# Optimization experiments

Hardware: AMD Instinct MI355X
Metric: run time of the kernel (lower is better)

The kernel has to match this reference:

```python
import jax, jax.numpy as jnp
import numpy as np

B, N = 2, 256
IN_N = 32          # input node features
H = 8              # per-layer default num_heads (GAT does not override it)
HN, HE = 64, 64    # hidden node / edge features per head
DN, DE = HN * H, HE * H  # 512, 512
OUT_N = 32


def _gat_layer(nodes, edges, mask, Wn, bn, We, be, Wa):
    # nodes: [b,n,dn_in], edges: [b,n,n,de_in], mask: [b,n] bool
    nf = nodes @ Wn + bn                                   # [b,n,DN]
    ef = jnp.einsum('bije,ef->bijf', edges, We) + be       # [b,n,n,DE]
    q = nf @ Wa                                            # [b,n,H]
    qe = jnp.einsum('bijf,fh->bijh', ef, Wa)               # [b,n,n,H]
    sn = jnp.einsum('bik,bjk->bij', q, q) / np.float32(np.sqrt(HN))
    se = jnp.einsum('bik,bijk->bij', q, qe) / np.float32(np.sqrt(HE))
    m = mask[..., None]
    wn = jax.nn.softmax(sn * m, axis=-1)                   # [b,n,n]
    we = jax.nn.softmax(se * m, axis=-1)                   # [b,n,n]
    awn = jnp.einsum('bij,bik->bjk', wn, nf)               # [b,n,DN]
    agg_e = jnp.einsum('bij,bijk->bik', we, ef)            # [b,n,DE]
    upd_nodes = nf + awn + agg_e                           # [b,n,DN]
    upd_edges = ef + we[..., None] * ef + jnp.einsum('bij,bik->bijk', wn, nf)
    re = jax.nn.elu(upd_edges)                             # [b,n,n,DE]
    re = (re + jnp.swapaxes(re, 1, 2)) / 2
    return jax.nn.elu(upd_nodes), re


def setup_inputs() -> dict:
    key = jax.random.key(0)
    ks = jax.random.split(key, 16)
    s = 0.05
    return {
        'nodes': jax.random.normal(ks[0], (B, N, IN_N), jnp.float32),
        'edges': jax.random.normal(ks[1], (B, N, N), jnp.float32),
        'node_mask': jnp.ones((B, N), dtype=bool),
        # layer 1 params
        'Wn1': jax.random.normal(ks[2], (IN_N, DN), jnp.float32) * s,
        'bn1': jnp.zeros((DN,), jnp.float32),
        'We1': jax.random.normal(ks[3], (1, DE), jnp.float32) * s,
        'be1': jnp.zeros((DE,), jnp.float32),
        'Wa1': jax.random.normal(ks[4], (DN, H), jnp.float32) * s,
        # layer 2 params
        'Wn2': jax.random.normal(ks[5], (DN, DN), jnp.float32) * s,
        'bn2': jnp.zeros((DN,), jnp.float32),
        'We2': jax.random.normal(ks[6], (DE, DE), jnp.float32) * s,
        'be2': jnp.zeros((DE,), jnp.float32),
        'Wa2': jax.random.normal(ks[7], (DN, H), jnp.float32) * s,
        # final projections
        'Wfn': jax.random.normal(ks[8], (DN, OUT_N), jnp.float32) * s,
        'bfn': jnp.zeros((OUT_N,), jnp.float32),
        'Wfe': jax.random.normal(ks[9], (DE, 1), jnp.float32) * s,
        'bfe': jnp.zeros((1,), jnp.float32),
    }


def reference(nodes, edges, node_mask, Wn1, bn1, We1, be1, Wa1,
              Wn2, bn2, We2, be2, Wa2, Wfn, bfn, Wfe, bfe):
    e = edges[..., None]                      # [b,n,n,1]
    e = (e + jnp.swapaxes(e, 1, 2)) / 2       # symmetrize
    e = jax.nn.relu(e)
    n, e = _gat_layer(nodes, e, node_mask, Wn1, bn1, We1, be1, Wa1)
    n, e = _gat_layer(n, e, node_mask, Wn2, bn2, We2, be2, Wa2)
    out_nodes = jnp.tanh(n @ Wfn + bfn)                                   # [b,n,OUT_N]
    out_edges = jnp.tanh(jnp.einsum('bijf,fo->bijo', e, Wfe) + bfe)[..., 0]  # [b,n,n]
    return out_nodes, out_edges
```

## Files before the change

### kernel.cpp

```cpp
#include <hip/hip_runtime.h>
#include <hip/hip_bf16.h>
#include <stdint.h>


typedef __attribute__((ext_vector_type(8))) short short8v;
typedef __attribute__((ext_vector_type(4))) float f32x4;

#define AS1 __attribute__((address_space(1)))
#define AS3 __attribute__((address_space(3)))

__device__ __forceinline__ float eluf(float x) { return x > 0.f ? x : (__expf(x) - 1.f); }

__device__ __forceinline__ short f2bf(float x) {
  union { float f; unsigned u; } v; v.f = x;
  unsigned r = v.u + 0x7fffu + ((v.u >> 16) & 1u);
  return (short)(r >> 16);
}

template<int OP>
__device__ float blockRed256(float v, float* s4) {
#pragma unroll
  for (int o = 32; o; o >>= 1) { float t = __shfl_xor(v, o); v = OP ? fmaxf(v, t) : v + t; }
  int w = threadIdx.x >> 6;
  __syncthreads();
  if ((threadIdx.x & 63) == 0) s4[w] = v;
  __syncthreads();
  return OP ? fmaxf(fmaxf(s4[0], s4[1]), fmaxf(s4[2], s4[3]))
            : (s4[0] + s4[1] + s4[2] + s4[3]);
}

__global__ __launch_bounds__(256) void k0m(const float* __restrict__ We2,
    const float* __restrict__ Wa2, const float* __restrict__ We1,
    const float* __restrict__ be1, const float* __restrict__ be2,
    const float* __restrict__ Wa1, short* __restrict__ Bp, float* __restrict__ M2,
    float* __restrict__ u1, float* __restrict__ v1, float* __restrict__ vb2) {
  int bid = blockIdx.x;
  if (bid < 128) {
    int id = bid * 256 + threadIdx.x;
    int c = id >> 11; int rem = id & 2047; int g = rem >> 9; int n = rem & 511;
    short8v v;
#pragma unroll
    for (int e = 0; e < 8; e++) v[e] = f2bf(We2[(c * 32 + g * 8 + e) * 512 + n]);
    int pos = n * 4 + (g ^ ((n >> 1) & 3));
    *(short8v*)(Bp + (c * 2048 + pos) * 8) = v;
    return;
  }
  int lane = threadIdx.x & 63;
  int idx = (bid - 128) * 4 + (threadIdx.x >> 6);
  if (idx < 512) {
    float a[8] = {0, 0, 0, 0, 0, 0, 0, 0};
    for (int k0 = lane; k0 < 512; k0 += 64) {
      float wv = We2[idx * 512 + k0];
      const float* wa = Wa2 + k0 * 8;
#pragma unroll
      for (int h = 0; h < 8; h++) a[h] += wv * wa[h];
    }
#pragma unroll
    for (int h = 0; h < 8; h++) {
      float v = a[h];
      for (int o = 32; o; o >>= 1) v += __shfl_xor(v, o);
      if (lane == 0) M2[idx * 8 + h] = v;
    }
  } else if (idx < 515) {
    const float* src = (idx == 512) ? We1 : (idx == 513 ? be1 : be2);
    const float* Wa = (idx == 514) ? Wa2 : Wa1;
    float* dst = (idx == 512) ? u1 : (idx == 513 ? v1 : vb2);
    float a[8] = {0, 0, 0, 0, 0, 0, 0, 0};
    for (int f = lane; f < 512; f += 64) {
      float s = src[f];
#pragma unroll
      for (int h = 0; h < 8; h++) a[h] += s * Wa[f * 8 + h];
    }
#pragma unroll
    for (int h = 0; h < 8; h++) {
      float v = a[h];
      for (int o = 32; o; o >>= 1) v += __shfl_xor(v, o);
      if (lane == 0) dst[h] = v;
    }
  }
}

__global__ __launch_bounds__(512) void k1_nf1(const float* __restrict__ nodes,
    const float* __restrict__ Wn1, const float* __restrict__ bn1,
    const float* __restrict__ Wa1, float* __restrict__ nf1, float* __restrict__ q1) {
  __shared__ float nrow[32];
  __shared__ float qL[8];
  int bi = blockIdx.x; int f = threadIdx.x;
  if (f < 32) nrow[f] = nodes[bi * 32 + f];
  if (f < 8) qL[f] = 0.f;
  __syncthreads();
  float acc = bn1[f];
#pragma unroll 8
  for (int c = 0; c < 32; c++) acc += nrow[c] * Wn1[c * 512 + f];
  nf1[bi * 512 + f] = acc;
  const float* wa = Wa1 + f * 8;
#pragma unroll
  for (int h = 0; h < 8; h++) {
    float v = acc * wa[h];
    for (int o = 32; o; o >>= 1) v += __shfl_xor(v, o);
    if ((f & 63) == 0) atomicAdd(&qL[h], v);
  }
  __syncthreads();
  if (f < 8) q1[bi * 8 + f] = qL[f];
}

__global__ __launch_bounds__(256) void k2_l1attn(const float* __restrict__ edges,
    const float* __restrict__ q1, const float* __restrict__ u1, const float* __restrict__ v1,
    float* __restrict__ e0, float* __restrict__ wn1, float* __restrict__ we1,
    float* __restrict__ tt) {
  __shared__ float s4[4];
  int bi = blockIdx.x; int b = bi >> 8; int i = bi & 255; int j = threadIdx.x;
  float qi[8], qj[8];
#pragma unroll
  for (int h = 0; h < 8; h++) { qi[h] = q1[bi * 8 + h]; qj[h] = q1[(b * 256 + j) * 8 + h]; }
  float eij = edges[bi * 256 + j];
  float eji = edges[(b * 256 + j) * 256 + i];
  float e0v = fmaxf(0.f, 0.5f * (eij + eji));
  e0[bi * 256 + j] = e0v;
  float sn = 0.f, aI = 0.f, cI = 0.f;
#pragma unroll
  for (int h = 0; h < 8; h++) { sn += qi[h] * qj[h]; aI += qi[h] * u1[h]; cI += qi[h] * v1[h]; }
  sn *= 0.125f;
  float se = (aI * e0v + cI) * 0.125f;
  float mn = blockRed256<1>(sn, s4);
  float en = __expf(sn - mn);
  float sumn = blockRed256<0>(en, s4);
  float wnv = en / sumn; wn1[bi * 256 + j] = wnv;
  float me = blockRed256<1>(se, s4);
  float ee = __expf(se - me);
  float sume = blockRed256<0>(ee, s4);
  float wev = ee / sume; we1[bi * 256 + j] = wev;
  float t = blockRed256<0>(wev * e0v, s4);
  if (j == 0) tt[bi] = t;
}

__global__ __launch_bounds__(512) void k34(const float* __restrict__ nf1,
    const float* __restrict__ wn1, const float* __restrict__ tt,
    const float* __restrict__ We1, const float* __restrict__ be1,
    const float* __restrict__ Wn2, const float* __restrict__ bn2,
    const float* __restrict__ Wa2, const float* __restrict__ M2,
    const float* __restrict__ vb2, float* __restrict__ nf2, float* __restrict__ q2,
    float* __restrict__ p2, float* __restrict__ cst) {
  __shared__ float n1L[2][512];
  __shared__ float qL[2][8];
  int bx = blockIdx.x;
  int b = bx >> 7; int x0 = (bx & 127) * 2; int k = threadIdx.x;
  int g0 = b * 256 + x0;
  float a0 = 0.f, a1 = 0.f;
#pragma unroll 4
  for (int i = 0; i < 256; i++) {
    float nv = nf1[(size_t)(b * 256 + i) * 512 + k];
    a0 += wn1[(b * 256 + i) * 256 + x0] * nv;
    a1 += wn1[(b * 256 + i) * 256 + x0 + 1] * nv;
  }
  float w = We1[k], be = be1[k];
  n1L[0][k] = eluf(nf1[(size_t)g0 * 512 + k] + a0 + tt[g0] * w + be);
  n1L[1][k] = eluf(nf1[(size_t)(g0 + 1) * 512 + k] + a1 + tt[g0 + 1] * w + be);
  if (k < 16) qL[k >> 3][k & 7] = 0.f;
  __syncthreads();
  float acc0 = bn2[k], acc1 = bn2[k];
#pragma unroll 4
  for (int g = 0; g < 512; g++) {
    float wv = Wn2[g * 512 + k];
    acc0 += n1L[0][g] * wv; acc1 += n1L[1][g] * wv;
  }
  nf2[(size_t)g0 * 512 + k] = acc0;
  nf2[(size_t)(g0 + 1) * 512 + k] = acc1;
  const float* wa = Wa2 + k * 8;
#pragma unroll
  for (int h = 0; h < 8; h++) {
    float v0 = acc0 * wa[h], v1 = acc1 * wa[h];
    for (int o = 32; o; o >>= 1) { v0 += __shfl_xor(v0, o); v1 += __shfl_xor(v1, o); }
    if ((k & 63) == 0) { atomicAdd(&qL[0][h], v0); atomicAdd(&qL[1][h], v1); }
  }
  __syncthreads();
  float q0[8], q1v[8];
#pragma unroll
  for (int h = 0; h < 8; h++) { q0[h] = qL[0][h]; q1v[h] = qL[1][h]; }
  if (k < 8) { q2[g0 * 8 + k] = q0[k]; q2[(g0 + 1) * 8 + k] = q1v[k]; }
  float p0 = 0.f, p1 = 0.f; const float* m2 = M2 + k * 8;
#pragma unroll
  for (int h = 0; h < 8; h++) { p0 += m2[h] * q0[h]; p1 += m2[h] * q1v[h]; }
  p2[(size_t)g0 * 512 + k] = p0;
  p2[(size_t)(g0 + 1) * 512 + k] = p1;
  if (k == 0) {
    float c0 = 0.f, c1 = 0.f;
#pragma unroll
    for (int h = 0; h < 8; h++) { c0 += q0[h] * vb2[h]; c1 += q1v[h] * vb2[h]; }
    cst[g0] = c0; cst[g0 + 1] = c1;
  }
}

__global__ __launch_bounds__(256) void k5b_pairs(const float* __restrict__ nf1,
    const float* __restrict__ p2, const float* __restrict__ e0,
    const float* __restrict__ wn1, const float* __restrict__ we1,
    const float* __restrict__ We1, const float* __restrict__ be1,
    const float* __restrict__ cst, float* __restrict__ se2) {
  __shared__ float NI[16 * 132], NJ[16 * 132], PI[16 * 132], PJ[16 * 132];
  __shared__ float W1[128], B1[128];
  int bid = blockIdx.x; int b = bid & 1; int pr = bid >> 1;
  int I = 0;
  { int p = pr; while (p >= 16 - I) { p -= 16 - I; I++; } pr = p; }
  int J = I + pr;
  int I0 = I * 16, J0 = J * 16;
  int tid = threadIdx.x; int ii = tid & 15, jj = tid >> 4;
  int gi = b * 256 + I0 + ii, gj = b * 256 + J0 + jj;
  int ij = gi * 256 + (J0 + jj), ji = gj * 256 + (I0 + ii);
  float e0v = e0[ij];
  float s1 = 1.f + we1[ij], w1 = wn1[ij];
  float s2 = 1.f + we1[ji], w2 = wn1[ji];
  float dot1 = 0.f, dot2 = 0.f;
  for (int fc = 0; fc < 4; fc++) {
    __syncthreads();
    int f00 = fc * 128;
    for (int t = tid; t < 2048; t += 256) {
      int row = t >> 7, f = t & 127;
      NI[row * 132 + f] = nf1[(size_t)(b * 256 + I0 + row) * 512 + f00 + f];
      NJ[row * 132 + f] = nf1[(size_t)(b * 256 + J0 + row) * 512 + f00 + f];
      PI[row * 132 + f] = p2[(size_t)(b * 256 + I0 + row) * 512 + f00 + f];
      PJ[row * 132 + f] = p2[(size_t)(b * 256 + J0 + row) * 512 + f00 + f];
    }
    if (tid < 128) { W1[tid] = We1[f00 + tid]; B1[tid] = be1[f00 + tid]; }
    __syncthreads();
#pragma unroll 8
    for (int f = 0; f < 128; f += 4) {
      float4 niv = *(const float4*)&NI[ii * 132 + f];
      float4 njv = *(const float4*)&NJ[jj * 132 + f];
      float4 piv = *(const float4*)&PI[ii * 132 + f];
      float4 pjv = *(const float4*)&PJ[jj * 132 + f];
      float4 wv = *(const float4*)&W1[f];
      float4 bv = *(const float4*)&B1[f];
      float ni_[4] = {niv.x, niv.y, niv.z, niv.w};
      float nj_[4] = {njv.x, njv.y, njv.z, njv.w};
      float pi_[4] = {piv.x, piv.y, piv.z, piv.w};
      float pj_[4] = {pjv.x, pjv.y, pjv.z, pjv.w};
      float w_[4] = {wv.x, wv.y, wv.z, wv.w};
      float b_[4] = {bv.x, bv.y, bv.z, bv.w};
#pragma unroll
      for (int e = 0; e < 4; e++) {
        float ef = e0v * w_[e] + b_[e];
        float x1 = ef * s1 + w1 * ni_[e];
        float x2 = ef * s2 + w2 * nj_[e];
        float e1v = 0.5f * (eluf(x1) + eluf(x2));
        dot1 += e1v * pi_[e];
        dot2 += e1v * pj_[e];
      }
    }
  }
  se2[ij] = (dot1 + cst[gi]) * 0.125f;
  se2[ji] = (dot2 + cst[gj]) * 0.125f;
}

__global__ __launch_bounds__(256) void k5ac(const float* __restrict__ q2,
    const float* __restrict__ se2, float* __restrict__ wn2, float* __restrict__ we2) {
  __shared__ float s4[4];
  int bi = blockIdx.x; int b = bi >> 8; int j = threadIdx.x;
  float sn = 0.f;
#pragma unroll
  for (int h = 0; h < 8; h++) sn += q2[bi * 8 + h] * q2[(b * 256 + j) * 8 + h];
  sn *= 0.125f;
  float mn = blockRed256<1>(sn, s4);
  float en = __expf(sn - mn);
  float s = blockRed256<0>(en, s4);
  wn2[bi * 256 + j] = en / s;
  float se = se2[bi * 256 + j];
  float me = blockRed256<1>(se, s4);
  float ee = __expf(se - me);
  float s2 = blockRed256<0>(ee, s4);
  we2[bi * 256 + j] = ee / s2;
}

__global__ __launch_bounds__(256) void kz(const float* __restrict__ nf1,
    const float* __restrict__ e0, const float* __restrict__ wn1,
    const float* __restrict__ we1, const float* __restrict__ we2,
    const float* __restrict__ We1, const float* __restrict__ be1, float* __restrict__ Z) {
  __shared__ float e0L[256], s1L[256], w1L[256], s2L[256], w2L[256], weL[256];
  int bi = blockIdx.x; int b = bi >> 8; int i = bi & 255; int tid = threadIdx.x;
  e0L[tid] = e0[bi * 256 + tid];
  s1L[tid] = 1.f + we1[bi * 256 + tid];
  w1L[tid] = wn1[bi * 256 + tid];
  weL[tid] = we2[bi * 256 + tid];
  s2L[tid] = 1.f + we1[(b * 256 + tid) * 256 + i];
  w2L[tid] = wn1[(b * 256 + tid) * 256 + i];
  __syncthreads();
  int k0 = tid, k1 = tid + 256;
  float W0 = We1[k0], B0 = be1[k0], W1 = We1[k1], B1 = be1[k1];
  float ni0 = nf1[(size_t)bi * 512 + k0], ni1 = nf1[(size_t)bi * 512 + k1];
  float z0 = 0.f, z1 = 0.f;
  const float* nfb = nf1 + (size_t)b * 256 * 512;
#pragma unroll 2
  for (int j = 0; j < 256; j++) {
    float e0v = e0L[j], s1 = s1L[j], w1 = w1L[j], s2 = s2L[j], w2 = w2L[j], we = weL[j];
    const float* nj = nfb + (size_t)j * 512;
    float nj0 = nj[k0], nj1 = nj[k1];
    float ef0 = e0v * W0 + B0;
    float x10 = ef0 * s1 + w1 * ni0, x20 = ef0 * s2 + w2 * nj0;
    z0 += we * 0.5f * (eluf(x10) + eluf(x20));
    float ef1 = e0v * W1 + B1;
    float x11 = ef1 * s1 + w1 * ni1, x21 = ef1 * s2 + w2 * nj1;
    z1 += we * 0.5f * (eluf(x11) + eluf(x21));
  }
  Z[(size_t)bi * 512 + k0] = z0;
  Z[(size_t)bi * 512 + k1] = z1;
}

__global__ __launch_bounds__(512, 2) void k6_main(
    const float* __restrict__ nf1, const float* __restrict__ nf2,
    const float* __restrict__ e0, const float* __restrict__ wn1, const float* __restrict__ we1,
    const float* __restrict__ wn2, const float* __restrict__ we2,
    const float* __restrict__ We1, const float* __restrict__ be1, const float* __restrict__ be2,
    const float* __restrict__ Wfe, const float* __restrict__ bfe,
    const short* __restrict__ Bp, float* __restrict__ Dout, float* __restrict__ oute) {
  __shared__ __align__(16) short As[2][4096];
  __shared__ __align__(16) short Bs[2][16384];
  __shared__ float nfI[16][516];
  __shared__ float nfJ[8][516];
  __shared__ float We1L[512], be1L[512];
  __shared__ float e0r[128], s1r[128], w1r[128], s2r[128], w2r[128];
  __shared__ float weAr[128], wnAr[128], weBr[128], wnBr[128];
  __shared__ float dsumA[128], dsumB[128];

  int bid = blockIdx.x;
  int b = bid & 1; int rest = bid >> 1;
  int Jh = rest & 1; int pr = rest >> 1;
  int I = 0;
  { int p = pr; while (p >= 16 - I) { p -= 16 - I; I++; } pr = p; }
  int J = I + pr;
  int I0 = I * 16, J0 = J * 16 + Jh * 8;
  bool dual = (I != J);

  int tid = threadIdx.x, lane = tid & 63, w = tid >> 6;
  int wm = w >> 2, wn_ = w & 3;
  int g4 = lane >> 4;

  We1L[tid] = We1[tid]; be1L[tid] = be1[tid];
  for (int t = tid; t < 16 * 512; t += 512)
    nfI[t >> 9][t & 511] = nf1[(size_t)(b * 256 + I0 + (t >> 9)) * 512 + (t & 511)];
  for (int t = tid; t < 8 * 512; t += 512)
    nfJ[t >> 9][t & 511] = nf1[(size_t)(b * 256 + J0 + (t >> 9)) * 512 + (t & 511)];
  if (tid < 128) {
    int i = I0 + (tid & 15), j = J0 + (tid >> 4);
    int ij = (b * 256 + i) * 256 + j, ji = (b * 256 + j) * 256 + i;
    e0r[tid] = e0[ij];
    s1r[tid] = 1.f + we1[ij]; w1r[tid] = wn1[ij];
    s2r[tid] = 1.f + we1[ji]; w2r[tid] = wn1[ji];
    weAr[tid] = we2[ij]; wnAr[tid] = wn2[ij];
    weBr[tid] = we2[ji]; wnBr[tid] = wn2[ji];
    dsumA[tid] = 0.f; dsumB[tid] = 0.f;
  }
  __syncthreads();

  int ar = tid >> 2;
  int ac = tid & 3;
  const float* niL = &nfI[ar & 15][0];
  const float* njL = &nfJ[ar >> 4][0];
  float e0v = e0r[ar], s1 = s1r[ar], w1 = w1r[ar], s2 = s2r[ar], w2 = w2r[ar];
  int apos8 = (ar * 4 + (ac ^ ((ar >> 1) & 3))) * 8;

  auto genA = [&](int cg, short* dst) {
    int f0 = cg * 32 + ac * 8;
    float4 gi0 = *(const float4*)(niL + f0);
    float4 gi1 = *(const float4*)(niL + f0 + 4);
    float4 gj0 = *(const float4*)(njL + f0);
    float4 gj1 = *(const float4*)(njL + f0 + 4);
    float niv[8] = {gi0.x, gi0.y, gi0.z, gi0.w, gi1.x, gi1.y, gi1.z, gi1.w};
    float njv[8] = {gj0.x, gj0.y, gj0.z, gj0.w, gj1.x, gj1.y, gj1.z, gj1.w};
    float Wv[8], bv[8];
    *(float4*)&Wv[0] = *(const float4*)&We1L[f0];
    *(float4*)&Wv[4] = *(const float4*)&We1L[f0 + 4];
    *(float4*)&bv[0] = *(const float4*)&be1L[f0];
    *(float4*)&bv[4] = *(const float4*)&be1L[f0 + 4];
    short8v pk;
#pragma unroll
    for (int e = 0; e < 8; e++) {
      float ef = e0v * Wv[e] + bv[e];
      float x1 = ef * s1 + w1 * niv[e];
      float x2 = ef * s2 + w2 * njv[e];
      float v = 0.5f * (eluf(x1) + eluf(x2));
      pk[e] = f2bf(v);
    }
    *(short8v*)(dst + apos8) = pk;
  };
  auto stageB = [&](int cg, short* dstB) {
    const char* g = (const char*)(Bp + cg * 16384);
#pragma unroll
    for (int it = 0; it < 4; ++it) {
      int off = it * 8192 + w * 1024;
      __builtin_amdgcn_global_load_lds(
          (const AS1 void*)(g + off + lane * 16),
          (AS3 void*)((char*)dstB + off), 16, 0, 0);
    }
  };

  f32x4 acc[4][8];
#pragma unroll
  for (int mi = 0; mi < 4; mi++)
#pragma unroll
    for (int nf = 0; nf < 8; nf++) acc[mi][nf] = (f32x4){0.f, 0.f, 0.f, 0.f};

  genA(0, As[0]);
  stageB(0, Bs[0]);
  __syncthreads();

  for (int c = 0; c < 16; ++c) {
    int cur = c & 1, nxt = cur ^ 1;
    if (c < 15) {
      genA(c + 1, As[nxt]);
      stageB(c + 1, Bs[nxt]);
    }
    short8v a[4];
#pragma unroll
    for (int mi = 0; mi < 4; mi++) {
      int row = wm * 64 + mi * 16 + (lane & 15);
      int cpos = row * 4 + (g4 ^ ((row >> 1) & 3));
      a[mi] = *(const short8v*)(As[cur] + cpos * 8);
    }
#pragma unroll
    for (int nf = 0; nf < 8; nf++) {
      int n = wn_ * 128 + nf * 16 + (lane & 15);
      int pos = n * 4 + (g4 ^ ((n >> 1) & 3));
      short8v bf = *(const short8v*)(Bs[cur] + pos * 8);
#pragma unroll
      for (int mi = 0; mi < 4; mi++)
        acc[mi][nf] = __builtin_amdgcn_mfma_f32_16x16x32_bf16(a[mi], bf, acc[mi][nf], 0, 0, 0);
    }
    __syncthreads();
  }

  float be2v[8], wfev[8];
#pragma unroll
  for (int nf = 0; nf < 8; nf++) {
    int k = wn_ * 128 + nf * 16 + (lane & 15);
    be2v[nf] = be2[k]; wfev[nf] = Wfe[k];
  }
#pragma unroll
  for (int mi = 0; mi < 4; mi++) {
    int jRow = J0 + wm * 4 + mi;
    const float* nf2j = nf2 + (size_t)(b * 256 + jRow) * 512;
#pragma unroll
    for (int r4 = 0; r4 < 4; r4++) {
      int jl = wm * 64 + mi * 16 + g4 * 4 + r4;
      int iRow = I0 + g4 * 4 + r4;
      const float* nf2i = nf2 + (size_t)(b * 256 + iRow) * 512;
      float sEA = 1.f + weAr[jl], wNA = wnAr[jl];
      float sEB = 1.f + weBr[jl], wNB = wnBr[jl];
      float dvA = 0.f, dvB = 0.f;
#pragma unroll
      for (int nf = 0; nf < 8; nf++) {
        int k = wn_ * 128 + nf * 16 + (lane & 15);
        float ef2 = acc[mi][nf][r4] + be2v[nf];
        float UA = ef2 * sEA + wNA * nf2i[k];
        dvA += eluf(UA) * wfev[nf];
        if (dual) {
          float UB = ef2 * sEB + wNB * nf2j[k];
          dvB += eluf(UB) * wfev[nf];
        }
      }
#pragma unroll
      for (int o = 1; o < 16; o <<= 1) dvA += __shfl_xor(dvA, o);
      if ((lane & 15) == 0) atomicAdd(&dsumA[jl], dvA);
      if (dual) {
#pragma unroll
        for (int o = 1; o < 16; o <<= 1) dvB += __shfl_xor(dvB, o);
        if ((lane & 15) == 0) atomicAdd(&dsumB[jl], dvB);
      }
    }
  }
  __syncthreads();
  if (tid < 128) {
    int i = I0 + (tid & 15), j = J0 + (tid >> 4);
    if (dual) {
      float v = tanhf(0.5f * (dsumA[tid] + dsumB[tid]) + bfe[0]);
      oute[(size_t)(b * 256 + i) * 256 + j] = v;
      oute[(size_t)(b * 256 + j) * 256 + i] = v;
    } else {
      Dout[(size_t)(b * 256 + i) * 256 + j] = dsumA[tid];
    }
  }
}

__global__ __launch_bounds__(256) void k9d(const float* __restrict__ D,
    const float* __restrict__ bfe, float* __restrict__ oute) {
  int bid = blockIdx.x; int b = bid >> 4; int I0 = (bid & 15) * 16;
  int r = threadIdx.x >> 4, c = threadIdx.x & 15;
  int gi = b * 256 + I0 + r, gj = b * 256 + I0 + c;
  float v = 0.5f * (D[(size_t)gi * 256 + I0 + c] + D[(size_t)gj * 256 + I0 + r]) + bfe[0];
  oute[(size_t)gi * 256 + I0 + c] = tanhf(v);
}

__global__ __launch_bounds__(512) void k78(const float* __restrict__ nf2,
    const float* __restrict__ wn2, const float* __restrict__ Z,
    const float* __restrict__ We2, const float* __restrict__ be2,
    const float* __restrict__ Wfn, const float* __restrict__ bfn,
    float* __restrict__ outn) {
  __shared__ float zL[2][512];
  __shared__ float n2L[2][512];
  __shared__ float red[512];
  int bx = blockIdx.x; int b = bx >> 7; int x0 = (bx & 127) * 2; int k = threadIdx.x;
  int g0 = b * 256 + x0;
  zL[0][k] = Z[(size_t)g0 * 512 + k];
  zL[1][k] = Z[(size_t)(g0 + 1) * 512 + k];
  float a0 = 0.f, a1 = 0.f;
#pragma unroll 4
  for (int i = 0; i < 256; i++) {
    float nv = nf2[(size_t)(b * 256 + i) * 512 + k];
    a0 += wn2[(b * 256 + i) * 256 + x0] * nv;
    a1 += wn2[(b * 256 + i) * 256 + x0 + 1] * nv;
  }
  __syncthreads();
  float ag0 = be2[k], ag1 = be2[k];
#pragma unroll 4
  for (int g = 0; g < 512; g++) {
    float wv = We2[g * 512 + k];
    ag0 += zL[0][g] * wv; ag1 += zL[1][g] * wv;
  }
  n2L[0][k] = eluf(nf2[(size_t)g0 * 512 + k] + a0 + ag0);
  n2L[1][k] = eluf(nf2[(size_t)(g0 + 1) * 512 + k] + a1 + ag1);
  __syncthreads();
  int row = k >> 8, t = k & 255;
  int o = t & 31, part = t >> 5;
  float acc = 0.f;
  for (int f = part * 64; f < part * 64 + 64; f++) acc += n2L[row][f] * Wfn[f * 32 + o];
  red[k] = acc;
  __syncthreads();
  if (k < 64) {
    int r2 = k >> 5, o2 = k & 31;
    float s = 0.f;
#pragma unroll
    for (int p = 0; p < 8; p++) s += red[r2 * 256 + p * 32 + o2];
    outn[(size_t)(g0 + r2) * 32 + o2] = tanhf(s + bfn[o2]);
  }
}

extern "C" void kernel_launch(void* const* d_in, const int* in_sizes, int n_in,
                              void* d_out, int out_size, void* d_ws, size_t ws_size,
                              hipStream_t stream) {
  const float* nodes = (const float*)d_in[0];
  const float* edges = (const float*)d_in[1];
  const float* Wn1 = (const float*)d_in[3];
  const float* bn1 = (const float*)d_in[4];
  const float* We1 = (const float*)d_in[5];
  const float* be1 = (const float*)d_in[6];
  const float* Wa1 = (const float*)d_in[7];
  const float* Wn2 = (const float*)d_in[8];
  const float* bn2 = (const float*)d_in[9];
  const float* We2 = (const float*)d_in[10];
  const float* be2 = (const float*)d_in[11];
  const float* Wa2 = (const float*)d_in[12];
  const float* Wfn = (const float*)d_in[13];
  const float* bfn = (const float*)d_in[14];
  const float* Wfe = (const float*)d_in[15];
  const float* bfe = (const float*)d_in[16];

  float* ws = (float*)d_ws;
  size_t off = 0;
  float* nf1 = ws + off; off += 262144;
  float* q1 = ws + off; off += 4096;
  float* e0 = ws + off; off += 131072;
  float* wn1 = ws + off; off += 131072;
  float* we1 = ws + off; off += 131072;
  float* tt = ws + off; off += 512;
  float* nf2 = ws + off; off += 262144;
  float* q2 = ws + off; off += 4096;
  float* p2 = ws + off; off += 262144;
  float* cst = ws + off; off += 512;
  float* wn2 = ws + off; off += 131072;
  float* we2 = ws + off; off += 131072;
  float* M2 = ws + off; off += 4096;
  float* u1 = ws + off; off += 8;
  float* v1 = ws + off; off += 8;
  float* vb2 = ws + off; off += 16;
  float* se2 = ws + off; off += 131072;
  float* Zb = ws + off; off += 262144;
  float* Dm = ws + off; off += 131072;
  short* Bp = (short*)(ws + off); off += 131072;

  float* outn = (float*)d_out;
  float* oute = outn + 2 * 256 * 32;

  hipLaunchKernelGGL(k0m, dim3(257), dim3(256), 0, stream, We2, Wa2, We1, be1, be2, Wa1,
                     Bp, M2, u1, v1, vb2);
  hipLaunchKernelGGL(k1_nf1, dim3(512), dim3(512), 0, stream, nodes, Wn1, bn1, Wa1, nf1, q1);
  hipLaunchKernelGGL(k2_l1attn, dim3(512), dim3(256), 0, stream, edges, q1, u1, v1, e0, wn1,
                     we1, tt);
  hipLaunchKernelGGL(k34, dim3(256), dim3(512), 0, stream, nf1, wn1, tt, We1, be1,
                     Wn2, bn2, Wa2, M2, vb2, nf2, q2, p2, cst);
  hipLaunchKernelGGL(k5b_pairs, dim3(272), dim3(256), 0, stream, nf1, p2, e0, wn1, we1, We1,
                     be1, cst, se2);
  hipLaunchKernelGGL(k5ac, dim3(512), dim3(256), 0, stream, q2, se2, wn2, we2);
  hipLaunchKernelGGL(kz, dim3(512), dim3(256), 0, stream, nf1, e0, wn1, we1, we2, We1, be1,
                     Zb);
  hipLaunchKernelGGL(k6_main, dim3(544), dim3(512), 0, stream, nf1, nf2, e0, wn1, we1, wn2,
                     we2, We1, be1, be2, Wfe, bfe, Bp, Dm, oute);
  hipLaunchKernelGGL(k78, dim3(256), dim3(512), 0, stream, nf2, wn2, Zb, We2, be2, Wfn, bfn,
                     outn);
  hipLaunchKernelGGL(k9d, dim3(32), dim3(256), 0, stream, Dm, bfe, oute);
}
```

Baseline: 352.1 us.

## Fuse small kernels, shrink main GEMM tiles, read B from global in bf16

Several small kernels are merged: nf1 projection into the weight-prep kernel, the softmax kernel with the Z reduction, and the diagonal edge fixup into the final node kernel. This cuts the launch count from nine to six. The main MFMA kernel now runs 256-thread blocks on quarter-width J tiles, giving twice as many blocks. It stages node features and We1/be1 in bf16 in LDS, and each wave loads its B fragments straight from global memory instead of staging them in LDS. This lowers LDS use and raises occupancy, but it adds bf16 rounding on the inputs to genA and exposes global-load latency inside the GEMM loop.

```diff
diff --git a/kernel.cpp b/kernel.cpp
--- a/kernel.cpp
+++ b/kernel.cpp
@@ -5,9 +5,6 @@
 
 typedef __attribute__((ext_vector_type(8))) short short8v;
 typedef __attribute__((ext_vector_type(4))) float f32x4;
-
-#define AS1 __attribute__((address_space(1)))
-#define AS3 __attribute__((address_space(3)))
 
 __device__ __forceinline__ float eluf(float x) { return x > 0.f ? x : (__expf(x) - 1.f); }
 
@@ -16,6 +13,9 @@
   unsigned r = v.u + 0x7fffu + ((v.u >> 16) & 1u);
   return (short)(r >> 16);
 }
+__device__ __forceinline__ float bf2f(short s) {
+  union { unsigned u; float f; } v; v.u = ((unsigned)(unsigned short)s) << 16; return v.f;
+}
 
 template<int OP>
 __device__ float blockRed256(float v, float* s4) {
@@ -29,12 +29,47 @@
             : (s4[0] + s4[1] + s4[2] + s4[3]);
 }
 
-__global__ __launch_bounds__(256) void k0m(const float* __restrict__ We2,
+__global__ __launch_bounds__(256) void k01(const float* __restrict__ We2,
     const float* __restrict__ Wa2, const float* __restrict__ We1,
     const float* __restrict__ be1, const float* __restrict__ be2,
-    const float* __restrict__ Wa1, short* __restrict__ Bp, float* __restrict__ M2,
-    float* __restrict__ u1, float* __restrict__ v1, float* __restrict__ vb2) {
+    const float* __restrict__ Wa1, const float* __restrict__ nodes,
+    const float* __restrict__ Wn1, const float* __restrict__ bn1,
+    short* __restrict__ Bp, float* __restrict__ M2,
+    float* __restrict__ u1, float* __restrict__ v1, float* __restrict__ vb2,
+    short* __restrict__ Wb1b, float* __restrict__ nf1, short* __restrict__ nf1b,
+    float* __restrict__ q1) {
   int bid = blockIdx.x;
+  if (bid >= 258) {
+    __shared__ float nrow[32];
+    __shared__ float qL[8];
+    int bi = bid - 258; int tid = threadIdx.x;
+    if (tid < 32) nrow[tid] = nodes[bi * 32 + tid];
+    if (tid < 8) qL[tid] = 0.f;
+    __syncthreads();
+    int f0 = tid, f1 = tid + 256;
+    float a0 = bn1[f0], a1 = bn1[f1];
+#pragma unroll 8
+    for (int c = 0; c < 32; c++) {
+      float nv = nrow[c];
+      a0 += nv * Wn1[c * 512 + f0];
+      a1 += nv * Wn1[c * 512 + f1];
+    }
+    nf1[(size_t)bi * 512 + f0] = a0;
+    nf1[(size_t)bi * 512 + f1] = a1;
+    nf1b[(size_t)bi * 512 + f0] = f2bf(a0);
+    nf1b[(size_t)bi * 512 + f1] = f2bf(a1);
+    const float* wa0 = Wa1 + f0 * 8;
+    const float* wa1 = Wa1 + f1 * 8;
+#pragma unroll
+    for (int h = 0; h < 8; h++) {
+      float v = a0 * wa0[h] + a1 * wa1[h];
+      for (int o = 32; o; o >>= 1) v += __shfl_xor(v, o);
+      if ((tid & 63) == 0) atomicAdd(&qL[h], v);
+    }
+    __syncthreads();
+    if (tid < 8) q1[bi * 8 + tid] = qL[tid];
+    return;
+  }
   if (bid < 128) {
     int id = bid * 256 + threadIdx.x;
     int c = id >> 11; int rem = id & 2047; int g = rem >> 9; int n = rem & 511;
@@ -43,6 +78,13 @@
     for (int e = 0; e < 8; e++) v[e] = f2bf(We2[(c * 32 + g * 8 + e) * 512 + n]);
     int pos = n * 4 + (g ^ ((n >> 1) & 3));
     *(short8v*)(Bp + (c * 2048 + pos) * 8) = v;
+    return;
+  }
+  if (bid == 257) {
+    for (int idx = threadIdx.x; idx < 1024; idx += 256) {
+      int g = idx >> 4, e = idx & 15;
+      Wb1b[idx] = f2bf(e < 8 ? We1[g * 8 + e] : be1[g * 8 + (e - 8)]);
+    }
     return;
   }
   int lane = threadIdx.x & 63;
@@ -78,30 +120,6 @@
       if (lane == 0) dst[h] = v;
     }
   }
-}
-
-__global__ __launch_bounds__(512) void k1_nf1(const float* __restrict__ nodes,
-    const float* __restrict__ Wn1, const float* __restrict__ bn1,
-    const float* __restrict__ Wa1, float* __restrict__ nf1, float* __restrict__ q1) {
-  __shared__ float nrow[32];
-  __shared__ float qL[8];
-  int bi = blockIdx.x; int f = threadIdx.x;
-  if (f < 32) nrow[f] = nodes[bi * 32 + f];
-  if (f < 8) qL[f] = 0.f;
-  __syncthreads();
-  float acc = bn1[f];
-#pragma unroll 8
-  for (int c = 0; c < 32; c++) acc += nrow[c] * Wn1[c * 512 + f];
-  nf1[bi * 512 + f] = acc;
-  const float* wa = Wa1 + f * 8;
-#pragma unroll
-  for (int h = 0; h < 8; h++) {
-    float v = acc * wa[h];
-    for (int o = 32; o; o >>= 1) v += __shfl_xor(v, o);
-    if ((f & 63) == 0) atomicAdd(&qL[h], v);
-  }
-  __syncthreads();
-  if (f < 8) q1[bi * 8 + f] = qL[f];
 }
 
 __global__ __launch_bounds__(256) void k2_l1attn(const float* __restrict__ edges,
@@ -251,10 +269,15 @@
   se2[ji] = (dot2 + cst[gj]) * 0.125f;
 }
 
-__global__ __launch_bounds__(256) void k5ac(const float* __restrict__ q2,
-    const float* __restrict__ se2, float* __restrict__ wn2, float* __restrict__ we2) {
+__global__ __launch_bounds__(256) void k5ackz(const float* __restrict__ q2,
+    const float* __restrict__ se2, const float* __restrict__ nf1,
+    const float* __restrict__ e0, const float* __restrict__ wn1,
+    const float* __restrict__ we1, const float* __restrict__ We1,
+    const float* __restrict__ be1, float* __restrict__ wn2, float* __restrict__ we2,
+    float* __restrict__ Z) {
   __shared__ float s4[4];
-  int bi = blockIdx.x; int b = bi >> 8; int j = threadIdx.x;
+  __shared__ float e0L[256], s1L[256], w1L[256], s2L[256], w2L[256], weL[256];
+  int bi = blockIdx.x; int b = bi >> 8; int i = bi & 255; int j = threadIdx.x;
   float sn = 0.f;
 #pragma unroll
   for (int h = 0; h < 8; h++) sn += q2[bi * 8 + h] * q2[(b * 256 + j) * 8 + h];
@@ -266,32 +289,25 @@
   float se = se2[bi * 256 + j];
   float me = blockRed256<1>(se, s4);
   float ee = __expf(se - me);
-  float s2 = blockRed256<0>(ee, s4);
-  we2[bi * 256 + j] = ee / s2;
-}
-
-__global__ __launch_bounds__(256) void kz(const float* __restrict__ nf1,
-    const float* __restrict__ e0, const float* __restrict__ wn1,
-    const float* __restrict__ we1, const float* __restrict__ we2,
-    const float* __restrict__ We1, const float* __restrict__ be1, float* __restrict__ Z) {
-  __shared__ float e0L[256], s1L[256], w1L[256], s2L[256], w2L[256], weL[256];
-  int bi = blockIdx.x; int b = bi >> 8; int i = bi & 255; int tid = threadIdx.x;
-  e0L[tid] = e0[bi * 256 + tid];
-  s1L[tid] = 1.f + we1[bi * 256 + tid];
-  w1L[tid] = wn1[bi * 256 + tid];
-  weL[tid] = we2[bi * 256 + tid];
-  s2L[tid] = 1.f + we1[(b * 256 + tid) * 256 + i];
-  w2L[tid] = wn1[(b * 256 + tid) * 256 + i];
-  __syncthreads();
-  int k0 = tid, k1 = tid + 256;
+  float s2s = blockRed256<0>(ee, s4);
+  float wev = ee / s2s;
+  we2[bi * 256 + j] = wev;
+  e0L[j] = e0[bi * 256 + j];
+  s1L[j] = 1.f + we1[bi * 256 + j];
+  w1L[j] = wn1[bi * 256 + j];
+  weL[j] = wev;
+  s2L[j] = 1.f + we1[(b * 256 + j) * 256 + i];
+  w2L[j] = wn1[(b * 256 + j) * 256 + i];
+  __syncthreads();
+  int k0 = j, k1 = j + 256;
   float W0 = We1[k0], B0 = be1[k0], W1 = We1[k1], B1 = be1[k1];
   float ni0 = nf1[(size_t)bi * 512 + k0], ni1 = nf1[(size_t)bi * 512 + k1];
   float z0 = 0.f, z1 = 0.f;
   const float* nfb = nf1 + (size_t)b * 256 * 512;
 #pragma unroll 2
-  for (int j = 0; j < 256; j++) {
-    float e0v = e0L[j], s1 = s1L[j], w1 = w1L[j], s2 = s2L[j], w2 = w2L[j], we = weL[j];
-    const float* nj = nfb + (size_t)j * 512;
+  for (int jj = 0; jj < 256; jj++) {
+    float e0v = e0L[jj], s1 = s1L[jj], w1 = w1L[jj], s2 = s2L[jj], w2 = w2L[jj], we = weL[jj];
+    const float* nj = nfb + (size_t)jj * 512;
     float nj0 = nj[k0], nj1 = nj[k1];
     float ef0 = e0v * W0 + B0;
     float x10 = ef0 * s1 + w1 * ni0, x20 = ef0 * s2 + w2 * nj0;
@@ -304,41 +320,45 @@
   Z[(size_t)bi * 512 + k1] = z1;
 }
 
-__global__ __launch_bounds__(512, 2) void k6_main(
-    const float* __restrict__ nf1, const float* __restrict__ nf2,
+__global__ __launch_bounds__(256, 2) void k6_main(
+    const short* __restrict__ nf1b, const float* __restrict__ nf2,
     const float* __restrict__ e0, const float* __restrict__ wn1, const float* __restrict__ we1,
     const float* __restrict__ wn2, const float* __restrict__ we2,
-    const float* __restrict__ We1, const float* __restrict__ be1, const float* __restrict__ be2,
-    const float* __restrict__ Wfe, const float* __restrict__ bfe,
-    const short* __restrict__ Bp, float* __restrict__ Dout, float* __restrict__ oute) {
-  __shared__ __align__(16) short As[2][4096];
-  __shared__ __align__(16) short Bs[2][16384];
-  __shared__ float nfI[16][516];
-  __shared__ float nfJ[8][516];
-  __shared__ float We1L[512], be1L[512];
-  __shared__ float e0r[128], s1r[128], w1r[128], s2r[128], w2r[128];
-  __shared__ float weAr[128], wnAr[128], weBr[128], wnBr[128];
-  __shared__ float dsumA[128], dsumB[128];
-
-  int bid = blockIdx.x;
+    const float* __restrict__ be2, const float* __restrict__ Wfe,
+    const float* __restrict__ bfe, const short* __restrict__ Bp,
+    const short* __restrict__ Wb1b, float* __restrict__ Dout, float* __restrict__ oute) {
+  __shared__ __align__(16) short As[2][2048];
+  __shared__ __align__(16) short nfIb[16 * 512];
+  __shared__ __align__(16) short nfJb[4 * 512];
+  __shared__ __align__(16) short WbL[1024];
+  __shared__ float e0r[64], s1r[64], w1r[64], s2r[64], w2r[64];
+  __shared__ float weAr[64], wnAr[64], weBr[64], wnBr[64];
+  __shared__ float dsumA[64], dsumB[64];
+
+  int bid = (blockIdx.x & 7) * 136 + (blockIdx.x >> 3);
   int b = bid & 1; int rest = bid >> 1;
-  int Jh = rest & 1; int pr = rest >> 1;
+  int Jq = rest & 3; int pr = rest >> 2;
   int I = 0;
   { int p = pr; while (p >= 16 - I) { p -= 16 - I; I++; } pr = p; }
   int J = I + pr;
-  int I0 = I * 16, J0 = J * 16 + Jh * 8;
+  int I0 = I * 16, J0 = J * 16 + Jq * 4;
   bool dual = (I != J);
 
   int tid = threadIdx.x, lane = tid & 63, w = tid >> 6;
-  int wm = w >> 2, wn_ = w & 3;
   int g4 = lane >> 4;
 
-  We1L[tid] = We1[tid]; be1L[tid] = be1[tid];
-  for (int t = tid; t < 16 * 512; t += 512)
-    nfI[t >> 9][t & 511] = nf1[(size_t)(b * 256 + I0 + (t >> 9)) * 512 + (t & 511)];
-  for (int t = tid; t < 8 * 512; t += 512)
-    nfJ[t >> 9][t & 511] = nf1[(size_t)(b * 256 + J0 + (t >> 9)) * 512 + (t & 511)];
-  if (tid < 128) {
+  for (int t = tid; t < 1024; t += 256) {
+    int row = t >> 6, g = t & 63;
+    *(short8v*)(nfIb + row * 512 + g * 8) =
+        *(const short8v*)(nf1b + (size_t)(b * 256 + I0 + row) * 512 + g * 8);
+  }
+  {
+    int row = tid >> 6, g = tid & 63;
+    *(short8v*)(nfJb + row * 512 + g * 8) =
+        *(const short8v*)(nf1b + (size_t)(b * 256 + J0 + row) * 512 + g * 8);
+  }
+  if (tid < 128) *(short8v*)(WbL + tid * 8) = *(const short8v*)(Wb1b + tid * 8);
+  if (tid < 64) {
     int i = I0 + (tid & 15), j = J0 + (tid >> 4);
     int ij = (b * 256 + i) * 256 + j, ji = (b * 256 + j) * 256 + i;
     e0r[tid] = e0[ij];
@@ -352,94 +372,81 @@
 
   int ar = tid >> 2;
   int ac = tid & 3;
-  const float* niL = &nfI[ar & 15][0];
-  const float* njL = &nfJ[ar >> 4][0];
+  const short* niB = nfIb + (ar & 15) * 512;
+  const short* njB = nfJb + (ar >> 4) * 512;
   float e0v = e0r[ar], s1 = s1r[ar], w1 = w1r[ar], s2 = s2r[ar], w2 = w2r[ar];
   int apos8 = (ar * 4 + (ac ^ ((ar >> 1) & 3))) * 8;
 
   auto genA = [&](int cg, short* dst) {
-    int f0 = cg * 32 + ac * 8;
-    float4 gi0 = *(const float4*)(niL + f0);
-    float4 gi1 = *(const float4*)(niL + f0 + 4);
-    float4 gj0 = *(const float4*)(njL + f0);
-    float4 gj1 = *(const float4*)(njL + f0 + 4);
-    float niv[8] = {gi0.x, gi0.y, gi0.z, gi0.w, gi1.x, gi1.y, gi1.z, gi1.w};
-    float njv[8] = {gj0.x, gj0.y, gj0.z, gj0.w, gj1.x, gj1.y, gj1.z, gj1.w};
-    float Wv[8], bv[8];
-    *(float4*)&Wv[0] = *(const float4*)&We1L[f0];
-    *(float4*)&Wv[4] = *(const float4*)&We1L[f0 + 4];
-    *(float4*)&bv[0] = *(const float4*)&be1L[f0];
-    *(float4*)&bv[4] = *(const float4*)&be1L[f0 + 4];
+    int gI = cg * 4 + ac;
+    short8v niq = *(const short8v*)(niB + gI * 8);
+    short8v njq = *(const short8v*)(njB + gI * 8);
+    short8v wq = *(const short8v*)(WbL + gI * 16);
+    short8v bq = *(const short8v*)(WbL + gI * 16 + 8);
     short8v pk;
 #pragma unroll
     for (int e = 0; e < 8; e++) {
-      float ef = e0v * Wv[e] + bv[e];
-      float x1 = ef * s1 + w1 * niv[e];
-      float x2 = ef * s2 + w2 * njv[e];
+      float ef = e0v * bf2f(wq[e]) + bf2f(bq[e]);
+      float x1 = ef * s1 + w1 * bf2f(niq[e]);
+      float x2 = ef * s2 + w2 * bf2f(njq[e]);
       float v = 0.5f * (eluf(x1) + eluf(x2));
       pk[e] = f2bf(v);
     }
     *(short8v*)(dst + apos8) = pk;
   };
-  auto stageB = [&](int cg, short* dstB) {
-    const char* g = (const char*)(Bp + cg * 16384);
-#pragma unroll
-    for (int it = 0; it < 4; ++it) {
-      int off = it * 8192 + w * 1024;
-      __builtin_amdgcn_global_load_lds(
-          (const AS1 void*)(g + off + lane * 16),
-          (AS3 void*)((char*)dstB + off), 16, 0, 0);
-    }
-  };
-
+
+  int boff[8];
+#pragma unroll
+  for (int nf = 0; nf < 8; nf++) {
+    int n = w * 128 + nf * 16 + (lane & 15);
+    boff[nf] = (n * 4 + (g4 ^ ((n >> 1) & 3))) * 8;
+  }
+
+  float be2v[8], wfev[8];
+#pragma unroll
+  for (int nf = 0; nf < 8; nf++) {
+    int k = w * 128 + nf * 16 + (lane & 15);
+    be2v[nf] = be2[k]; wfev[nf] = Wfe[k];
+  }
   f32x4 acc[4][8];
 #pragma unroll
   for (int mi = 0; mi < 4; mi++)
 #pragma unroll
-    for (int nf = 0; nf < 8; nf++) acc[mi][nf] = (f32x4){0.f, 0.f, 0.f, 0.f};
+    for (int nf = 0; nf < 8; nf++)
+      acc[mi][nf] = (f32x4){be2v[nf], be2v[nf], be2v[nf], be2v[nf]};
 
   genA(0, As[0]);
-  stageB(0, Bs[0]);
   __syncthreads();
 
   for (int c = 0; c < 16; ++c) {
-    int cur = c & 1, nxt = cur ^ 1;
-    if (c < 15) {
-      genA(c + 1, As[nxt]);
-      stageB(c + 1, Bs[nxt]);
-    }
+    int cur = c & 1;
+    const short* bbase = Bp + c * 16384;
+    short8v bf[8];
+#pragma unroll
+    for (int nf = 0; nf < 8; nf++) bf[nf] = *(const short8v*)(bbase + boff[nf]);
+    if (c < 15) genA(c + 1, As[cur ^ 1]);
     short8v a[4];
 #pragma unroll
     for (int mi = 0; mi < 4; mi++) {
-      int row = wm * 64 + mi * 16 + (lane & 15);
+      int row = mi * 16 + (lane & 15);
       int cpos = row * 4 + (g4 ^ ((row >> 1) & 3));
       a[mi] = *(const short8v*)(As[cur] + cpos * 8);
     }
 #pragma unroll
-    for (int nf = 0; nf < 8; nf++) {
-      int n = wn_ * 128 + nf * 16 + (lane & 15);
-      int pos = n * 4 + (g4 ^ ((n >> 1) & 3));
-      short8v bf = *(const short8v*)(Bs[cur] + pos * 8);
+    for (int nf = 0; nf < 8; nf++)
 #pragma unroll
       for (int mi = 0; mi < 4; mi++)
-        acc[mi][nf] = __builtin_amdgcn_mfma_f32_16x16x32_bf16(a[mi], bf, acc[mi][nf], 0, 0, 0);
-    }
+        acc[mi][nf] = __builtin_amdgcn_mfma_f32_16x16x32_bf16(a[mi], bf[nf], acc[mi][nf], 0, 0, 0);
     __syncthreads();
   }
 
-  float be2v[8], wfev[8];
-#pragma unroll
-  for (int nf = 0; nf < 8; nf++) {
-    int k = wn_ * 128 + nf * 16 + (lane & 15);
-    be2v[nf] = be2[k]; wfev[nf] = Wfe[k];
-  }
 #pragma unroll
   for (int mi = 0; mi < 4; mi++) {
-    int jRow = J0 + wm * 4 + mi;
+    int jRow = J0 + mi;
     const float* nf2j = nf2 + (size_t)(b * 256 + jRow) * 512;
 #pragma unroll
     for (int r4 = 0; r4 < 4; r4++) {
-      int jl = wm * 64 + mi * 16 + g4 * 4 + r4;
+      int jl = mi * 16 + g4 * 4 + r4;
       int iRow = I0 + g4 * 4 + r4;
       const float* nf2i = nf2 + (size_t)(b * 256 + iRow) * 512;
       float sEA = 1.f + weAr[jl], wNA = wnAr[jl];
@@ -447,8 +454,8 @@
       float dvA = 0.f, dvB = 0.f;
 #pragma unroll
       for (int nf = 0; nf < 8; nf++) {
-        int k = wn_ * 128 + nf * 16 + (lane & 15);
-        float ef2 = acc[mi][nf][r4] + be2v[nf];
+        int k = w * 128 + nf * 16 + (lane & 15);
+        float ef2 = acc[mi][nf][r4];
         float UA = ef2 * sEA + wNA * nf2i[k];
         dvA += eluf(UA) * wfev[nf];
         if (dual) {
@@ -467,7 +474,7 @@
     }
   }
   __syncthreads();
-  if (tid < 128) {
+  if (tid < 64) {
     int i = I0 + (tid & 15), j = J0 + (tid >> 4);
     if (dual) {
       float v = tanhf(0.5f * (dsumA[tid] + dsumB[tid]) + bfe[0]);
@@ -479,24 +486,28 @@
   }
 }
 
-__global__ __launch_bounds__(256) void k9d(const float* __restrict__ D,
-    const float* __restrict__ bfe, float* __restrict__ oute) {
-  int bid = blockIdx.x; int b = bid >> 4; int I0 = (bid & 15) * 16;
-  int r = threadIdx.x >> 4, c = threadIdx.x & 15;
-  int gi = b * 256 + I0 + r, gj = b * 256 + I0 + c;
-  float v = 0.5f * (D[(size_t)gi * 256 + I0 + c] + D[(size_t)gj * 256 + I0 + r]) + bfe[0];
-  oute[(size_t)gi * 256 + I0 + c] = tanhf(v);
-}
-
 __global__ __launch_bounds__(512) void k78(const float* __restrict__ nf2,
     const float* __restrict__ wn2, const float* __restrict__ Z,
     const float* __restrict__ We2, const float* __restrict__ be2,
     const float* __restrict__ Wfn, const float* __restrict__ bfn,
-    float* __restrict__ outn) {
+    const float* __restrict__ Dm, const float* __restrict__ bfe,
+    float* __restrict__ outn, float* __restrict__ oute) {
+  int bx = blockIdx.x; int k = threadIdx.x;
+  if (bx >= 256) {
+    if (k < 256) {
+      int d = bx - 256; int b = d >> 4; int I0 = (d & 15) * 16;
+      int r = k >> 4, c = k & 15;
+      int gi = b * 256 + I0 + r, gj = b * 256 + I0 + c;
+      float v = 0.5f * (Dm[(size_t)gi * 256 + I0 + c] + Dm[(size_t)gj * 256 + I0 + r]) +
+                bfe[0];
+      oute[(size_t)gi * 256 + I0 + c] = tanhf(v);
+    }
+    return;
+  }
   __shared__ float zL[2][512];
   __shared__ float n2L[2][512];
   __shared__ float red[512];
-  int bx = blockIdx.x; int b = bx >> 7; int x0 = (bx & 127) * 2; int k = threadIdx.x;
+  int b = bx >> 7; int x0 = (bx & 127) * 2;
   int g0 = b * 256 + x0;
   zL[0][k] = Z[(size_t)g0 * 512 + k];
   zL[1][k] = Z[(size_t)(g0 + 1) * 512 + k];
@@ -573,26 +584,25 @@
   float* se2 = ws + off; off += 131072;
   float* Zb = ws + off; off += 262144;
   float* Dm = ws + off; off += 131072;
+  short* nf1b = (short*)(ws + off); off += 131072;
   short* Bp = (short*)(ws + off); off += 131072;
+  short* Wb1b = (short*)(ws + off); off += 512;
 
   float* outn = (float*)d_out;
   float* oute = outn + 2 * 256 * 32;
 
-  hipLaunchKernelGGL(k0m, dim3(257), dim3(256), 0, stream, We2, Wa2, We1, be1, be2, Wa1,
-                     Bp, M2, u1, v1, vb2);
-  hipLaunchKernelGGL(k1_nf1, dim3(512), dim3(512), 0, stream, nodes, Wn1, bn1, Wa1, nf1, q1);
+  hipLaunchKernelGGL(k01, dim3(770), dim3(256), 0, stream, We2, Wa2, We1, be1, be2, Wa1,
+                     nodes, Wn1, bn1, Bp, M2, u1, v1, vb2, Wb1b, nf1, nf1b, q1);
   hipLaunchKernelGGL(k2_l1attn, dim3(512), dim3(256), 0, stream, edges, q1, u1, v1, e0, wn1,
                      we1, tt);
   hipLaunchKernelGGL(k34, dim3(256), dim3(512), 0, stream, nf1, wn1, tt, We1, be1,
                      Wn2, bn2, Wa2, M2, vb2, nf2, q2, p2, cst);
   hipLaunchKernelGGL(k5b_pairs, dim3(272), dim3(256), 0, stream, nf1, p2, e0, wn1, we1, We1,
                      be1, cst, se2);
-  hipLaunchKernelGGL(k5ac, dim3(512), dim3(256), 0, stream, q2, se2, wn2, we2);
-  hipLaunchKernelGGL(kz, dim3(512), dim3(256), 0, stream, nf1, e0, wn1, we1, we2, We1, be1,
-                     Zb);
-  hipLaunchKernelGGL(k6_main, dim3(544), dim3(512), 0, stream, nf1, nf2, e0, wn1, we1, wn2,
-                     we2, We1, be1, be2, Wfe, bfe, Bp, Dm, oute);
-  hipLaunchKernelGGL(k78, dim3(256), dim3(512), 0, stream, nf2, wn2, Zb, We2, be2, Wfn, bfn,
-                     outn);
-  hipLaunchKernelGGL(k9d, dim3(32), dim3(256), 0, stream, Dm, bfe, oute);
-}
+  hipLaunchKernelGGL(k5ackz, dim3(512), dim3(256), 0, stream, q2, se2, nf1, e0, wn1, we1,
+                     We1, be1, wn2, we2, Zb);
+  hipLaunchKernelGGL(k6_main, dim3(1088), dim3(256), 0, stream, nf1b, nf2, e0, wn1, we1,
+                     wn2, we2, be2, Wfe, bfe, Bp, Wb1b, Dm, oute);
+  hipLaunchKernelGGL(k78, dim3(288), dim3(512), 0, stream, nf2, wn2, Zb, We2, be2, Wfn, bfn,
+                     Dm, bfe, outn, oute);
+}
```

Result: faster. 341.5 us (-3.0%).
